# Optimization experiments

Measured on AMD Instinct MI355X. Metric: run time of the kernel, lower is better.

Reference implementation:

```python
import jax, jax.numpy as jnp
import numpy as np

N, E, HDIM, NG = 10000, 320000, 256, 20
BN_EPS = 1e-5


def setup_inputs() -> dict:
    key = jax.random.key(0)
    ks = jax.random.split(key, 12)
    inp = {
        "x": jax.random.normal(ks[0], (N, HDIM), dtype=jnp.float32),
        "rbf": jax.random.uniform(ks[1], (E, NG), dtype=jnp.float32),
        "ei": jax.random.randint(ks[2], (2, E), 0, N, dtype=jnp.int64),
        # filter_net: Linear(n_g, hdim) -> SiLU -> Linear(hdim, hdim)
        "Wf1": jax.random.normal(ks[3], (NG, HDIM), dtype=jnp.float32) / np.sqrt(NG),
        "bf1": jnp.zeros((HDIM,), dtype=jnp.float32),
        "Wf2": jax.random.normal(ks[4], (HDIM, HDIM), dtype=jnp.float32) / np.sqrt(HDIM),
        "bf2": jnp.zeros((HDIM,), dtype=jnp.float32),
        # node_update: Linear(hdim, hdim) -> SiLU -> Linear(hdim, hdim)
        "Wu1": jax.random.normal(ks[5], (HDIM, HDIM), dtype=jnp.float32) / np.sqrt(HDIM),
        "bu1": jnp.zeros((HDIM,), dtype=jnp.float32),
        "Wu2": jax.random.normal(ks[6], (HDIM, HDIM), dtype=jnp.float32) / np.sqrt(HDIM),
        "bu2": jnp.zeros((HDIM,), dtype=jnp.float32),
        # BatchNorm1d affine params
        "gamma": jnp.ones((HDIM,), dtype=jnp.float32),
        "beta": jnp.zeros((HDIM,), dtype=jnp.float32),
    }
    return inp


def reference(x, rbf, Wf1, bf1, Wf2, bf2, Wu1, bu1, Wu2, bu2, gamma, beta, ei):
    row, col = ei[0], ei[1]
    # filter_net(rbf): [E, hdim]
    filt = jax.nn.silu(rbf @ Wf1 + bf1) @ Wf2 + bf2
    # message = gather(x, col) * filter
    msg = x[col] * filt  # [E, hdim]
    # scatter_add aggregation over destination nodes
    agg = jax.ops.segment_sum(msg, row, num_segments=x.shape[0])  # [N, hdim]
    # node_update MLP
    h = jax.nn.silu(agg @ Wu1 + bu1) @ Wu2 + bu2  # [N, hdim]
    # BatchNorm1d (training mode: batch stats, biased variance)
    mean = jnp.mean(h, axis=0)
    var = jnp.mean(jnp.square(h - mean), axis=0)
    bn = gamma * (h - mean) * jax.lax.rsqrt(var + BN_EPS) + beta
    return x + bn
```

## Files before the change

### kernel.cpp

```cpp
#include <hip/hip_runtime.h>

#define N_NODES 10000
#define E_EDGES 320000
#define HDIM    256
#define NG      20
#define BN_EPS  1e-5f

typedef __attribute__((ext_vector_type(8))) short short8;
typedef __attribute__((ext_vector_type(4))) float f32x4;

__device__ __forceinline__ float silu_f(float v) {
    float e = __expf(-v);
    return v * __builtin_amdgcn_rcpf(1.0f + e);
}

__device__ __forceinline__ unsigned int cvt_pk(float lo, float hi) {
    unsigned int r;
    asm("v_cvt_pk_bf16_f32 %0, %1, %2" : "=v"(r) : "v"(lo), "v"(hi));
    return r;
}

__device__ __forceinline__ unsigned short f2bf(float f) {
    union { float f; unsigned int u; } v; v.f = f;
    unsigned int r = v.u + 0x7fffu + ((v.u >> 16) & 1u);
    return (unsigned short)(r >> 16);
}

__device__ __forceinline__ f32x4 bf4_to_f32(uint2 u) {
    union { unsigned int i; float f; } a, b, c, d;
    a.i = u.x << 16; b.i = u.x & 0xFFFF0000u;
    c.i = u.y << 16; d.i = u.y & 0xFFFF0000u;
    return (f32x4){a.f, b.f, c.f, d.f};
}

__global__ __launch_bounds__(256) void prep_hist_kernel(
    const float* __restrict__ Wf2, const float* __restrict__ Wu1,
    const float* __restrict__ Wu2, const float* __restrict__ Wf1,
    const float* __restrict__ bf1, const int* __restrict__ ei_row,
    const float* __restrict__ x,
    unsigned short* __restrict__ Pf2, unsigned short* __restrict__ Pu1,
    unsigned short* __restrict__ Pu2, unsigned short* __restrict__ P1,
    int* __restrict__ cnt, unsigned short* __restrict__ xb)
{
    const int bx = blockIdx.x;
    if (bx >= 2050) {
        const int idx = ((bx - 2050) * 256 + threadIdx.x) * 8;
        const float4* s = (const float4*)(x + idx);
        float4 a = s[0], b = s[1];
        *(uint4*)(xb + idx) = make_uint4(cvt_pk(a.x, a.y), cvt_pk(a.z, a.w),
                                         cvt_pk(b.x, b.y), cvt_pk(b.z, b.w));
        return;
    }
    if (bx >= 800) {
        int e = (bx - 800) * 256 + threadIdx.x;
        atomicAdd(&cnt[ei_row[e]], 1);
        return;
    }
    int tid = bx * 256 + threadIdx.x;
    if (tid < 196608) {
        int which = tid >> 16, local = tid & 65535;
        const float* W = (which == 0) ? Wf2 : (which == 1) ? Wu1 : Wu2;
        unsigned short* P = (which == 0) ? Pf2 : (which == 1) ? Pu1 : Pu2;
        int j = local & 7, lane = (local >> 3) & 63;
        int ntile = (local >> 9) & 15, kstep = local >> 13;
        int k = kstep * 32 + (lane >> 4) * 8 + j;
        int n = ntile * 16 + (lane & 15);
        P[local] = f2bf(W[k * 256 + n]);
    } else {
        int local = tid - 196608;
        int j = local & 7, lane = (local >> 3) & 63, ntile = local >> 9;
        int k = (lane >> 4) * 8 + j;
        int n = ntile * 16 + (lane & 15);
        float v = (k < NG) ? Wf1[k * 256 + n] : (k == NG ? bf1[n] : 0.0f);
        P1[local] = f2bf(v);
    }
}

__global__ __launch_bounds__(256) void scan_kernel(int* __restrict__ cnt) {
    __shared__ int tot[256];
    const int t = threadIdx.x;
    int loc[40];
    int s = 0;
    #pragma unroll
    for (int i = 0; i < 40; ++i) { loc[i] = cnt[t * 40 + i]; s += loc[i]; }
    tot[t] = s;
    __syncthreads();
    for (int off = 1; off < 256; off <<= 1) {
        int u = (t >= off) ? tot[t - off] : 0;
        __syncthreads();
        tot[t] += u;
        __syncthreads();
    }
    int pre = tot[t] - s;
    #pragma unroll
    for (int i = 0; i < 40; ++i) { int v = loc[i]; cnt[t * 40 + i] = pre; pre += v; }
}

__global__ __launch_bounds__(256) void fill_kernel(const int* __restrict__ ei_row,
                                                   int* __restrict__ cnt,
                                                   int* __restrict__ perm,
                                                   int* __restrict__ nodepos) {
    int e = blockIdx.x * 256 + threadIdx.x;
    int r = ei_row[e];
    int pos = atomicAdd(&cnt[r], 1);
    perm[pos] = e;
    nodepos[pos] = r;
}

#define SM_NID 0
#define SM_COL 256
#define SM_RBF 512
#define SM_HID 5632
#define SM_TOT 38400

__global__ __launch_bounds__(256, 4) void edge_kernel(
    const float* __restrict__ rbf, const int* __restrict__ ei_col,
    const int* __restrict__ perm, const int* __restrict__ nodepos,
    const unsigned short* __restrict__ P1, const unsigned short* __restrict__ P2,
    const float* __restrict__ bf2, const unsigned short* __restrict__ xb,
    float* __restrict__ agg)
{
    __shared__ char sm[SM_TOT];
    int* nid_s = (int*)(sm + SM_NID);
    int* col_s = (int*)(sm + SM_COL);

    const int t = threadIdx.x;
    int blk = blockIdx.x;
    blk = (blk & 7) * 625 + (blk >> 3);
    const int p0 = blk * 64;
    const int l = t & 63, w = t >> 6;
    const int l15 = l & 15, l4 = l >> 4;

    if (t < 64) {
        nid_s[t] = nodepos[p0 + t];
        col_s[t] = ei_col[perm[p0 + t]];
    }
    if (t < 128) {
        const int row = t >> 1, half = t & 1;
        const float* rp = rbf + (size_t)perm[p0 + row] * NG + half * 10;
        float v[10];
        if (half == 0) {
            float4 a = *(const float4*)rp, b = *(const float4*)(rp + 4);
            float2 c = *(const float2*)(rp + 8);
            v[0]=a.x; v[1]=a.y; v[2]=a.z; v[3]=a.w; v[4]=b.x;
            v[5]=b.y; v[6]=b.z; v[7]=b.w; v[8]=c.x; v[9]=c.y;
        } else {
            float2 a = *(const float2*)rp;
            float4 b = *(const float4*)(rp + 2), c = *(const float4*)(rp + 6);
            v[0]=a.x; v[1]=a.y; v[2]=b.x; v[3]=b.y; v[4]=b.z;
            v[5]=b.w; v[6]=c.x; v[7]=c.y; v[8]=c.z; v[9]=c.w;
        }
        unsigned int* dst = (unsigned int*)(sm + SM_RBF + row * 80 + half * 20);
        #pragma unroll
        for (int i = 0; i < 5; ++i) dst[i] = cvt_pk(v[2*i], v[2*i+1]);
    } else if (t < 192) {
        const int row = t - 128;
        *(unsigned long long*)(sm + SM_RBF + row * 80 + 40) = 0x3F80ull;
        *(uint4*)(sm + SM_RBF + row * 80 + 48) = make_uint4(0, 0, 0, 0);
    }

    short8 a1[4], acur[4];
    #pragma unroll
    for (int mt = 0; mt < 4; ++mt) {
        a1[mt]   = *(const short8*)(P1 + ((4 * w + mt) * 64 + l) * 8);
        acur[mt] = *(const short8*)(P2 + ((4 * w + mt) * 64 + l) * 8);
    }

    __syncthreads();

    f32x4 acc[4][4];
    #pragma unroll
    for (int mt = 0; mt < 4; ++mt)
        #pragma unroll
        for (int nt = 0; nt < 4; ++nt) acc[mt][nt] = (f32x4)0.0f;

    #pragma unroll
    for (int nt = 0; nt < 4; ++nt) {
        short8 bfr = *(const short8*)(sm + SM_RBF + (nt * 16 + l15) * 80 + l4 * 16);
        #pragma unroll
        for (int mt = 0; mt < 4; ++mt)
            acc[mt][nt] = __builtin_amdgcn_mfma_f32_16x16x32_bf16(a1[mt], bfr, acc[mt][nt], 0, 0, 0);
    }

    #pragma unroll
    for (int mt = 0; mt < 4; ++mt) {
        const int hc0 = w * 64 + mt * 16 + l4 * 4;
        #pragma unroll
        for (int nt = 0; nt < 4; ++nt) {
            const int row = nt * 16 + l15;
            unsigned int pk0 = cvt_pk(silu_f(acc[mt][nt][0]), silu_f(acc[mt][nt][1]));
            unsigned int pk1 = cvt_pk(silu_f(acc[mt][nt][2]), silu_f(acc[mt][nt][3]));
            *(uint2*)(sm + SM_HID + row * 512 +
                      (((hc0 >> 3) ^ (row & 7)) << 4) + (hc0 & 7) * 2) =
                make_uint2(pk0, pk1);
        }
    }
    __syncthreads();

    #pragma unroll
    for (int mt = 0; mt < 4; ++mt)
        #pragma unroll
        for (int nt = 0; nt < 4; ++nt) acc[mt][nt] = (f32x4)0.0f;

    for (int ks = 0; ks < 8; ++ks) {
        short8 anext[4];
        if (ks < 7) {
            #pragma unroll
            for (int mt = 0; mt < 4; ++mt)
                anext[mt] = *(const short8*)(P2 + (((ks + 1) * 16 + 4 * w + mt) * 64 + l) * 8);
        }
        #pragma unroll
        for (int nt = 0; nt < 4; ++nt) {
            const int row = nt * 16 + l15;
            short8 bfh = *(const short8*)(sm + SM_HID + row * 512 +
                            ((((ks << 2) + l4) ^ (row & 7)) << 4));
            #pragma unroll
            for (int mt = 0; mt < 4; ++mt)
                acc[mt][nt] = __builtin_amdgcn_mfma_f32_16x16x32_bf16(acur[mt], bfh, acc[mt][nt], 0, 0, 0);
        }
        if (ks < 7) {
            #pragma unroll
            for (int mt = 0; mt < 4; ++mt) acur[mt] = anext[mt];
        }
    }
    __syncthreads();

    f32x4 bc4[4];
    #pragma unroll
    for (int mt = 0; mt < 4; ++mt)
        bc4[mt] = *(const f32x4*)(bf2 + w * 64 + mt * 16 + l4 * 4);

    const unsigned short* xbase[4];
    #pragma unroll
    for (int nt = 0; nt < 4; ++nt)
        xbase[nt] = xb + (size_t)col_s[nt * 16 + l15] * HDIM;

    float sum = 0.0f;
    int cur = nid_s[0];

    {
        uint2 xp[8];
        #pragma unroll
        for (int mt = 0; mt < 4; ++mt) {
            const int fc0 = w * 64 + mt * 16 + l4 * 4;
            xp[mt]     = *(const uint2*)(xbase[0] + fc0);
            xp[4 + mt] = *(const uint2*)(xbase[1] + fc0);
        }
        #pragma unroll
        for (int ni = 0; ni < 2; ++ni) {
            const int pos = ni * 16 + l15;
            #pragma unroll
            for (int mt = 0; mt < 4; ++mt) {
                const int fc0 = w * 64 + mt * 16 + l4 * 4;
                f32x4 mv = (acc[mt][ni] + bc4[mt]) * bf4_to_f32(xp[ni * 4 + mt]);
                *(f32x4*)(sm + SM_HID + pos * 1024 + (((fc0 >> 2) ^ (pos & 7)) << 4)) = mv;
            }
        }
    }
    uint2 xq[8];
    #pragma unroll
    for (int mt = 0; mt < 4; ++mt) {
        const int fc0 = w * 64 + mt * 16 + l4 * 4;
        xq[mt]     = *(const uint2*)(xbase[2] + fc0);
        xq[4 + mt] = *(const uint2*)(xbase[3] + fc0);
    }
    __syncthreads();
    for (int pos = 0; pos < 32; ++pos) {
        const int nid = nid_s[pos];
        float v = *(const float*)(sm + SM_HID + pos * 1024 +
                    (((t >> 2) ^ (pos & 7)) << 4) + (t & 3) * 4);
        if (nid != cur) {
            atomicAdd(&agg[(size_t)cur * HDIM + t], sum);
            sum = 0.0f; cur = nid;
        }
        sum += v;
    }
    __syncthreads();

    #pragma unroll
    for (int ni = 0; ni < 2; ++ni) {
        const int nt  = 2 + ni;
        const int pos = ni * 16 + l15;
        #pragma unroll
        for (int mt = 0; mt < 4; ++mt) {
            const int fc0 = w * 64 + mt * 16 + l4 * 4;
            f32x4 mv = (acc[mt][nt] + bc4[mt]) * bf4_to_f32(xq[ni * 4 + mt]);
            *(f32x4*)(sm + SM_HID + pos * 1024 + (((fc0 >> 2) ^ (pos & 7)) << 4)) = mv;
        }
    }
    __syncthreads();
    for (int pos = 0; pos < 32; ++pos) {
        const int nid = nid_s[32 + pos];
        float v = *(const float*)(sm + SM_HID + pos * 1024 +
                    (((t >> 2) ^ (pos & 7)) << 4) + (t & 3) * 4);
        if (nid != cur) {
            atomicAdd(&agg[(size_t)cur * HDIM + t], sum);
            sum = 0.0f; cur = nid;
        }
        sum += v;
    }
    atomicAdd(&agg[(size_t)cur * HDIM + t], sum);
}

__global__ __launch_bounds__(256, 3) void node_kernel(
    const float* __restrict__ agg, const float* __restrict__ bu1,
    const float* __restrict__ bu2,
    const unsigned short* __restrict__ Pu1, const unsigned short* __restrict__ Pu2,
    float* __restrict__ hout, float* __restrict__ sums)
{
    __shared__ char sm[32768];
    const int t  = threadIdx.x;
    const int r0 = blockIdx.x * 64;
    const int l = t & 63, w = t >> 6;
    const int l15 = l & 15, l4 = l >> 4;

    {
        const int row = t & 63, q = t >> 6;
        const bool valid = (r0 + row) < N_NODES;
        const float4* src = (const float4*)(agg + (size_t)(r0 + row) * HDIM) + q * 16;
        #pragma unroll
        for (int i = 0; i < 16; ++i) {
            float4 v = valid ? src[i] : make_float4(0.f, 0.f, 0.f, 0.f);
            const int c0 = q * 64 + i * 4;
            *(uint2*)(sm + row * 512 + (((c0 >> 3) ^ (row & 7)) << 4) + (c0 & 7) * 2) =
                make_uint2(cvt_pk(v.x, v.y), cvt_pk(v.z, v.w));
        }
    }

    short8 acur[4];
    #pragma unroll
    for (int mt = 0; mt < 4; ++mt)
        acur[mt] = *(const short8*)(Pu1 + ((4 * w + mt) * 64 + l) * 8);

    __syncthreads();

    f32x4 acc[4][4];
    #pragma unroll
    for (int mt = 0; mt < 4; ++mt)
        #pragma unroll
        for (int nt = 0; nt < 4; ++nt) acc[mt][nt] = (f32x4)0.0f;

    for (int ks = 0; ks < 8; ++ks) {
        short8 anext[4];
        if (ks < 7) {
            #pragma unroll
            for (int mt = 0; mt < 4; ++mt)
                anext[mt] = *(const short8*)(Pu1 + (((ks + 1) * 16 + 4 * w + mt) * 64 + l) * 8);
        }
        #pragma unroll
        for (int nt = 0; nt < 4; ++nt) {
            const int row = nt * 16 + l15;
            short8 bfa = *(const short8*)(sm + row * 512 +
                            ((((ks << 2) + l4) ^ (row & 7)) << 4));
            #pragma unroll
            for (int mt = 0; mt < 4; ++mt)
                acc[mt][nt] = __builtin_amdgcn_mfma_f32_16x16x32_bf16(acur[mt], bfa, acc[mt][nt], 0, 0, 0);
        }
        if (ks < 7) {
            #pragma unroll
            for (int mt = 0; mt < 4; ++mt) acur[mt] = anext[mt];
        }
    }
    __syncthreads();

    #pragma unroll
    for (int mt = 0; mt < 4; ++mt)
        acur[mt] = *(const short8*)(Pu2 + ((4 * w + mt) * 64 + l) * 8);

    #pragma unroll
    for (int mt = 0; mt < 4; ++mt) {
        const int mc0 = w * 64 + mt * 16 + l4 * 4;
        f32x4 b4 = *(const f32x4*)(bu1 + mc0);
        #pragma unroll
        for (int nt = 0; nt < 4; ++nt) {
            const int row = nt * 16 + l15;
            unsigned int pk0 = cvt_pk(silu_f(acc[mt][nt][0] + b4[0]), silu_f(acc[mt][nt][1] + b4[1]));
            unsigned int pk1 = cvt_pk(silu_f(acc[mt][nt][2] + b4[2]), silu_f(acc[mt][nt][3] + b4[3]));
            *(uint2*)(sm + row * 512 + (((mc0 >> 3) ^ (row & 7)) << 4) + (mc0 & 7) * 2) =
                make_uint2(pk0, pk1);
            acc[mt][nt] = (f32x4)0.0f;
        }
    }
    __syncthreads();

    for (int ks = 0; ks < 8; ++ks) {
        short8 anext[4];
        if (ks < 7) {
            #pragma unroll
            for (int mt = 0; mt < 4; ++mt)
                anext[mt] = *(const short8*)(Pu2 + (((ks + 1) * 16 + 4 * w + mt) * 64 + l) * 8);
        }
        #pragma unroll
        for (int nt = 0; nt < 4; ++nt) {
            const int row = nt * 16 + l15;
            short8 bfm = *(const short8*)(sm + row * 512 +
                            ((((ks << 2) + l4) ^ (row & 7)) << 4));
            #pragma unroll
            for (int mt = 0; mt < 4; ++mt)
                acc[mt][nt] = __builtin_amdgcn_mfma_f32_16x16x32_bf16(acur[mt], bfm, acc[mt][nt], 0, 0, 0);
        }
        if (ks < 7) {
            #pragma unroll
            for (int mt = 0; mt < 4; ++mt) acur[mt] = anext[mt];
        }
    }

    #pragma unroll
    for (int mt = 0; mt < 4; ++mt) {
        const int hc0 = w * 64 + mt * 16 + l4 * 4;
        f32x4 b4 = *(const f32x4*)(bu2 + hc0);
        f32x4 s = (f32x4)0.0f, s2 = (f32x4)0.0f;
        #pragma unroll
        for (int nt = 0; nt < 4; ++nt) {
            const int gr = r0 + nt * 16 + l15;
            if (gr < N_NODES) {
                f32x4 hv = acc[mt][nt] + b4;
                *(f32x4*)(hout + (size_t)gr * HDIM + hc0) = hv;
                s += hv; s2 += hv * hv;
            }
        }
        #pragma unroll
        for (int off = 1; off < 16; off <<= 1) {
            #pragma unroll
            for (int r = 0; r < 4; ++r) {
                s[r]  += __shfl_xor(s[r], off);
                s2[r] += __shfl_xor(s2[r], off);
            }
        }
        if (l15 == 0) {
            #pragma unroll
            for (int r = 0; r < 4; ++r) {
                atomicAdd(&sums[hc0 + r], s[r]);
                atomicAdd(&sums[HDIM + hc0 + r], s2[r]);
            }
        }
    }
}

__global__ __launch_bounds__(256) void final_kernel(
    const float* __restrict__ x, const float* __restrict__ sums,
    const float* __restrict__ gamma, const float* __restrict__ beta,
    float* __restrict__ out)
{
    const int i4 = blockIdx.x * 256 + threadIdx.x;
    const int j  = (i4 & 63) * 4;
    f32x4 mean = *(const f32x4*)(sums + j) * (1.0f / N_NODES);
    f32x4 s2   = *(const f32x4*)(sums + HDIM + j) * (1.0f / N_NODES);
    f32x4 g    = *(const f32x4*)(gamma + j);
    f32x4 b    = *(const f32x4*)(beta + j);
    f32x4 hv   = ((f32x4*)out)[i4];
    f32x4 xv   = ((const f32x4*)x)[i4];
    f32x4 var  = s2 - mean * mean;
    f32x4 inv;
    #pragma unroll
    for (int r = 0; r < 4; ++r) inv[r] = rsqrtf(var[r] + BN_EPS);
    ((f32x4*)out)[i4] = xv + g * (hv - mean) * inv + b;
}

extern "C" void kernel_launch(void* const* d_in, const int* in_sizes, int n_in,
                              void* d_out, int out_size, void* d_ws, size_t ws_size,
                              hipStream_t stream) {
    const float* x     = (const float*)d_in[0];
    const float* rbf   = (const float*)d_in[1];
    const int*   ei    = (const int*)d_in[2];
    const float* Wf1   = (const float*)d_in[3];
    const float* bf1   = (const float*)d_in[4];
    const float* Wf2   = (const float*)d_in[5];
    const float* bf2   = (const float*)d_in[6];
    const float* Wu1   = (const float*)d_in[7];
    const float* bu1   = (const float*)d_in[8];
    const float* Wu2   = (const float*)d_in[9];
    const float* bu2   = (const float*)d_in[10];
    const float* gamma = (const float*)d_in[11];
    const float* beta  = (const float*)d_in[12];
    float* out = (float*)d_out;

    char* ws = (char*)d_ws;
    float* agg     = (float*)(ws);
    float* sums    = (float*)(ws + 10240000);
    int*   cnt     = (int*)(ws + 10242048);
    int*   perm    = (int*)(ws + 10283008);
    int*   nodepos = (int*)(ws + 11563008);
    unsigned short* Pf2 = (unsigned short*)(ws + 12843008);
    unsigned short* Pu1 = (unsigned short*)(ws + 12974080);
    unsigned short* Pu2 = (unsigned short*)(ws + 13105152);
    unsigned short* P1  = (unsigned short*)(ws + 13236224);

    unsigned short* xb = (unsigned short*)d_out;

    hipMemsetAsync(agg, 0, 10283008, stream);

    prep_hist_kernel<<<3300, 256, 0, stream>>>(Wf2, Wu1, Wu2, Wf1, bf1, ei, x,
                                               Pf2, Pu1, Pu2, P1, cnt, xb);
    scan_kernel<<<1, 256, 0, stream>>>(cnt);
    fill_kernel<<<E_EDGES / 256, 256, 0, stream>>>(ei, cnt, perm, nodepos);

    edge_kernel<<<E_EDGES / 64, 256, 0, stream>>>(
        rbf, ei + E_EDGES, perm, nodepos, P1, Pf2, bf2, xb, agg);
    node_kernel<<<(N_NODES + 63) / 64, 256, 0, stream>>>(
        agg, bu1, bu2, Pu1, Pu2, out, sums);
    final_kernel<<<(N_NODES * HDIM / 4) / 256, 256, 0, stream>>>(
        x, sums, gamma, beta, out);
}
```

Before: 196.5 us.

## Split edge kernel across 8 waves, precompute permuted cols, bf16 message staging

The edge kernel now runs 512 threads per 64-edge block, with each wave owning 32 output channels instead of 64. This halves per-thread accumulators and is meant to raise occupancy and latency hiding. The fill kernel additionally writes a permuted column array (stored in the output buffer's unused tail), which removes the dependent perm→col gather chain. Messages are staged to LDS as bf16 in one pass, so the segmented reduction runs once over all 64 edges instead of in two halves. Storing messages in bf16 before summing adds rounding error to the aggregation.

```diff
diff --git a/kernel.cpp b/kernel.cpp
--- a/kernel.cpp
+++ b/kernel.cpp
@@ -97,32 +97,34 @@
 }
 
 __global__ __launch_bounds__(256) void fill_kernel(const int* __restrict__ ei_row,
+                                                   const int* __restrict__ ei_col,
                                                    int* __restrict__ cnt,
                                                    int* __restrict__ perm,
-                                                   int* __restrict__ nodepos) {
+                                                   int* __restrict__ nodepos,
+                                                   int* __restrict__ colperm) {
     int e = blockIdx.x * 256 + threadIdx.x;
     int r = ei_row[e];
+    int c = ei_col[e];
     int pos = atomicAdd(&cnt[r], 1);
     perm[pos] = e;
     nodepos[pos] = r;
+    colperm[pos] = c;
 }
 
 #define SM_NID 0
-#define SM_COL 256
-#define SM_RBF 512
-#define SM_HID 5632
-#define SM_TOT 38400
-
-__global__ __launch_bounds__(256, 4) void edge_kernel(
-    const float* __restrict__ rbf, const int* __restrict__ ei_col,
-    const int* __restrict__ perm, const int* __restrict__ nodepos,
+#define SM_RBF 256
+#define SM_HID 5376
+#define SM_TOT 38144
+
+__global__ __launch_bounds__(512, 6) void edge_kernel(
+    const float* __restrict__ rbf, const int* __restrict__ perm,
+    const int* __restrict__ nodepos, const int* __restrict__ colperm,
     const unsigned short* __restrict__ P1, const unsigned short* __restrict__ P2,
     const float* __restrict__ bf2, const unsigned short* __restrict__ xb,
     float* __restrict__ agg)
 {
     __shared__ char sm[SM_TOT];
     int* nid_s = (int*)(sm + SM_NID);
-    int* col_s = (int*)(sm + SM_COL);
 
     const int t = threadIdx.x;
     int blk = blockIdx.x;
@@ -131,10 +133,7 @@
     const int l = t & 63, w = t >> 6;
     const int l15 = l & 15, l4 = l >> 4;
 
-    if (t < 64) {
-        nid_s[t] = nodepos[p0 + t];
-        col_s[t] = ei_col[perm[p0 + t]];
-    }
+    if (t < 64) nid_s[t] = nodepos[p0 + t];
     if (t < 128) {
         const int row = t >> 1, half = t & 1;
         const float* rp = rbf + (size_t)perm[p0 + row] * NG + half * 10;
@@ -159,18 +158,22 @@
         *(uint4*)(sm + SM_RBF + row * 80 + 48) = make_uint4(0, 0, 0, 0);
     }
 
-    short8 a1[4], acur[4];
-    #pragma unroll
-    for (int mt = 0; mt < 4; ++mt) {
-        a1[mt]   = *(const short8*)(P1 + ((4 * w + mt) * 64 + l) * 8);
-        acur[mt] = *(const short8*)(P2 + ((4 * w + mt) * 64 + l) * 8);
-    }
-
-    __syncthreads();
-
-    f32x4 acc[4][4];
-    #pragma unroll
-    for (int mt = 0; mt < 4; ++mt)
+    int colp[4];
+    #pragma unroll
+    for (int nt = 0; nt < 4; ++nt) colp[nt] = colperm[p0 + nt * 16 + l15];
+
+    short8 a1[2], acur[2];
+    #pragma unroll
+    for (int mt = 0; mt < 2; ++mt) {
+        a1[mt]   = *(const short8*)(P1 + ((2 * w + mt) * 64 + l) * 8);
+        acur[mt] = *(const short8*)(P2 + ((2 * w + mt) * 64 + l) * 8);
+    }
+
+    __syncthreads();
+
+    f32x4 acc[2][4];
+    #pragma unroll
+    for (int mt = 0; mt < 2; ++mt)
         #pragma unroll
         for (int nt = 0; nt < 4; ++nt) acc[mt][nt] = (f32x4)0.0f;
 
@@ -178,13 +181,13 @@
     for (int nt = 0; nt < 4; ++nt) {
         short8 bfr = *(const short8*)(sm + SM_RBF + (nt * 16 + l15) * 80 + l4 * 16);
         #pragma unroll
-        for (int mt = 0; mt < 4; ++mt)
+        for (int mt = 0; mt < 2; ++mt)
             acc[mt][nt] = __builtin_amdgcn_mfma_f32_16x16x32_bf16(a1[mt], bfr, acc[mt][nt], 0, 0, 0);
     }
 
     #pragma unroll
-    for (int mt = 0; mt < 4; ++mt) {
-        const int hc0 = w * 64 + mt * 16 + l4 * 4;
+    for (int mt = 0; mt < 2; ++mt) {
+        const int hc0 = w * 32 + mt * 16 + l4 * 4;
         #pragma unroll
         for (int nt = 0; nt < 4; ++nt) {
             const int row = nt * 16 + l15;
@@ -198,16 +201,16 @@
     __syncthreads();
 
     #pragma unroll
-    for (int mt = 0; mt < 4; ++mt)
+    for (int mt = 0; mt < 2; ++mt)
         #pragma unroll
         for (int nt = 0; nt < 4; ++nt) acc[mt][nt] = (f32x4)0.0f;
 
     for (int ks = 0; ks < 8; ++ks) {
-        short8 anext[4];
-        if (ks < 7) {
-            #pragma unroll
-            for (int mt = 0; mt < 4; ++mt)
-                anext[mt] = *(const short8*)(P2 + (((ks + 1) * 16 + 4 * w + mt) * 64 + l) * 8);
+        short8 anext[2];
+        if (ks < 7) {
+            #pragma unroll
+            for (int mt = 0; mt < 2; ++mt)
+                anext[mt] = *(const short8*)(P2 + (((ks + 1) * 16 + 2 * w + mt) * 64 + l) * 8);
         }
         #pragma unroll
         for (int nt = 0; nt < 4; ++nt) {
@@ -215,91 +218,61 @@
             short8 bfh = *(const short8*)(sm + SM_HID + row * 512 +
                             ((((ks << 2) + l4) ^ (row & 7)) << 4));
             #pragma unroll
-            for (int mt = 0; mt < 4; ++mt)
+            for (int mt = 0; mt < 2; ++mt)
                 acc[mt][nt] = __builtin_amdgcn_mfma_f32_16x16x32_bf16(acur[mt], bfh, acc[mt][nt], 0, 0, 0);
         }
         if (ks < 7) {
             #pragma unroll
-            for (int mt = 0; mt < 4; ++mt) acur[mt] = anext[mt];
-        }
-    }
-    __syncthreads();
-
-    f32x4 bc4[4];
-    #pragma unroll
-    for (int mt = 0; mt < 4; ++mt)
-        bc4[mt] = *(const f32x4*)(bf2 + w * 64 + mt * 16 + l4 * 4);
-
-    const unsigned short* xbase[4];
-    #pragma unroll
-    for (int nt = 0; nt < 4; ++nt)
-        xbase[nt] = xb + (size_t)col_s[nt * 16 + l15] * HDIM;
-
-    float sum = 0.0f;
-    int cur = nid_s[0];
-
-    {
-        uint2 xp[8];
-        #pragma unroll
-        for (int mt = 0; mt < 4; ++mt) {
-            const int fc0 = w * 64 + mt * 16 + l4 * 4;
-            xp[mt]     = *(const uint2*)(xbase[0] + fc0);
-            xp[4 + mt] = *(const uint2*)(xbase[1] + fc0);
-        }
-        #pragma unroll
-        for (int ni = 0; ni < 2; ++ni) {
-            const int pos = ni * 16 + l15;
-            #pragma unroll
-            for (int mt = 0; mt < 4; ++mt) {
-                const int fc0 = w * 64 + mt * 16 + l4 * 4;
-                f32x4 mv = (acc[mt][ni] + bc4[mt]) * bf4_to_f32(xp[ni * 4 + mt]);
-                *(f32x4*)(sm + SM_HID + pos * 1024 + (((fc0 >> 2) ^ (pos & 7)) << 4)) = mv;
+            for (int mt = 0; mt < 2; ++mt) acur[mt] = anext[mt];
+        }
+    }
+
+    uint2 xv[2][4];
+    #pragma unroll
+    for (int mt = 0; mt < 2; ++mt) {
+        const int fc0 = w * 32 + mt * 16 + l4 * 4;
+        #pragma unroll
+        for (int nt = 0; nt < 4; ++nt)
+            xv[mt][nt] = *(const uint2*)(xb + (size_t)colp[nt] * HDIM + fc0);
+    }
+
+    f32x4 bc2[2];
+    #pragma unroll
+    for (int mt = 0; mt < 2; ++mt)
+        bc2[mt] = *(const f32x4*)(bf2 + w * 32 + mt * 16 + l4 * 4);
+
+    __syncthreads();
+
+    #pragma unroll
+    for (int mt = 0; mt < 2; ++mt) {
+        const int fc0 = w * 32 + mt * 16 + l4 * 4;
+        #pragma unroll
+        for (int nt = 0; nt < 4; ++nt) {
+            const int row = nt * 16 + l15;
+            f32x4 m = (acc[mt][nt] + bc2[mt]) * bf4_to_f32(xv[mt][nt]);
+            *(uint2*)(sm + SM_HID + row * 512 +
+                      (((fc0 >> 3) ^ (row & 7)) << 4) + (fc0 & 7) * 2) =
+                make_uint2(cvt_pk(m[0], m[1]), cvt_pk(m[2], m[3]));
+        }
+    }
+    __syncthreads();
+
+    if (t < 256) {
+        float sum = 0.0f;
+        int cur = nid_s[0];
+        for (int pos = 0; pos < 64; ++pos) {
+            const int nid = nid_s[pos];
+            unsigned short u = *(const unsigned short*)(sm + SM_HID + pos * 512 +
+                                (((t >> 3) ^ (pos & 7)) << 4) + (t & 7) * 2);
+            union { unsigned int i; float f; } cv; cv.i = ((unsigned int)u) << 16;
+            if (nid != cur) {
+                atomicAdd(&agg[(size_t)cur * HDIM + t], sum);
+                sum = 0.0f; cur = nid;
             }
-        }
-    }
-    uint2 xq[8];
-    #pragma unroll
-    for (int mt = 0; mt < 4; ++mt) {
-        const int fc0 = w * 64 + mt * 16 + l4 * 4;
-        xq[mt]     = *(const uint2*)(xbase[2] + fc0);
-        xq[4 + mt] = *(const uint2*)(xbase[3] + fc0);
-    }
-    __syncthreads();
-    for (int pos = 0; pos < 32; ++pos) {
-        const int nid = nid_s[pos];
-        float v = *(const float*)(sm + SM_HID + pos * 1024 +
-                    (((t >> 2) ^ (pos & 7)) << 4) + (t & 3) * 4);
-        if (nid != cur) {
-            atomicAdd(&agg[(size_t)cur * HDIM + t], sum);
-            sum = 0.0f; cur = nid;
-        }
-        sum += v;
-    }
-    __syncthreads();
-
-    #pragma unroll
-    for (int ni = 0; ni < 2; ++ni) {
-        const int nt  = 2 + ni;
-        const int pos = ni * 16 + l15;
-        #pragma unroll
-        for (int mt = 0; mt < 4; ++mt) {
-            const int fc0 = w * 64 + mt * 16 + l4 * 4;
-            f32x4 mv = (acc[mt][nt] + bc4[mt]) * bf4_to_f32(xq[ni * 4 + mt]);
-            *(f32x4*)(sm + SM_HID + pos * 1024 + (((fc0 >> 2) ^ (pos & 7)) << 4)) = mv;
-        }
-    }
-    __syncthreads();
-    for (int pos = 0; pos < 32; ++pos) {
-        const int nid = nid_s[32 + pos];
-        float v = *(const float*)(sm + SM_HID + pos * 1024 +
-                    (((t >> 2) ^ (pos & 7)) << 4) + (t & 3) * 4);
-        if (nid != cur) {
-            atomicAdd(&agg[(size_t)cur * HDIM + t], sum);
-            sum = 0.0f; cur = nid;
-        }
-        sum += v;
-    }
-    atomicAdd(&agg[(size_t)cur * HDIM + t], sum);
+            sum += cv.f;
+        }
+        atomicAdd(&agg[(size_t)cur * HDIM + t], sum);
+    }
 }
 
 __global__ __launch_bounds__(256, 3) void node_kernel(
@@ -487,16 +460,18 @@
     unsigned short* P1  = (unsigned short*)(ws + 13236224);
 
     unsigned short* xb = (unsigned short*)d_out;
+    int* colperm = (int*)((char*)d_out + 5120000);
 
     hipMemsetAsync(agg, 0, 10283008, stream);
 
     prep_hist_kernel<<<3300, 256, 0, stream>>>(Wf2, Wu1, Wu2, Wf1, bf1, ei, x,
                                                Pf2, Pu1, Pu2, P1, cnt, xb);
     scan_kernel<<<1, 256, 0, stream>>>(cnt);
-    fill_kernel<<<E_EDGES / 256, 256, 0, stream>>>(ei, cnt, perm, nodepos);
-
-    edge_kernel<<<E_EDGES / 64, 256, 0, stream>>>(
-        rbf, ei + E_EDGES, perm, nodepos, P1, Pf2, bf2, xb, agg);
+    fill_kernel<<<E_EDGES / 256, 256, 0, stream>>>(ei, ei + E_EDGES, cnt,
+                                                   perm, nodepos, colperm);
+
+    edge_kernel<<<E_EDGES / 64, 512, 0, stream>>>(
+        rbf, perm, nodepos, colperm, P1, Pf2, bf2, xb, agg);
     node_kernel<<<(N_NODES + 63) / 64, 256, 0, stream>>>(
         agg, bu1, bu2, Pu1, Pu2, out, sums);
     final_kernel<<<(N_NODES * HDIM / 4) / 256, 256, 0, stream>>>(
```

Measured after the change: 199.1 us. About the same (+1.4%).
